# Kernel optimization log

Measured on AMD Instinct MI355X. Metric: run time of the kernel, lower is better.

Reference implementation:

```python
import jax, jax.numpy as jnp
import numpy as np

B, H1, H2, D, V1 = 4, 512, 640, 640, 1025  # V1 = vocab_size + 1 (blank)
T, U = 256, 128


def setup_inputs() -> dict:
    key = jax.random.key(0)
    ks = jax.random.split(key, 8)
    s = lambda fan_in: 1.0 / np.sqrt(fan_in)
    return {
        "encoder_outputs": jax.random.normal(ks[0], (B, H1, T), jnp.float32),
        "predictor_outputs": jax.random.normal(ks[1], (B, H2, U), jnp.float32),
        # Linear weights stored as [in, out]
        "W_enc": jax.random.uniform(ks[2], (H1, D), jnp.float32, -s(H1), s(H1)),
        "b_enc": jax.random.uniform(ks[3], (D,), jnp.float32, -s(H1), s(H1)),
        "W_pred": jax.random.uniform(ks[4], (H2, D), jnp.float32, -s(H2), s(H2)),
        "b_pred": jax.random.uniform(ks[5], (D,), jnp.float32, -s(H2), s(H2)),
        "W_out": jax.random.uniform(ks[6], (D, V1), jnp.float32, -s(D), s(D)),
        "b_out": jax.random.uniform(ks[7], (V1,), jnp.float32, -s(D), s(D)),
    }


def reference(encoder_outputs, predictor_outputs, W_enc, b_enc, W_pred, b_pred, W_out, b_out):
    # transpose(1,2): [B,H1,T] -> [B,T,H1], [B,H2,U] -> [B,U,H2], fused into einsum
    f = jnp.einsum("bht,hd->btd", encoder_outputs, W_enc) + b_enc   # [B,T,D]
    g = jnp.einsum("bhu,hd->bud", predictor_outputs, W_pred) + b_pred  # [B,U,D]
    h = jax.nn.relu(f[:, :, None, :] + g[:, None, :, :])            # [B,T,U,D]
    logits = jnp.einsum("btud,dv->btuv", h, W_out) + b_out          # [B,T,U,V+1]
    return jax.nn.log_softmax(logits, axis=-1)
```

## Files before the change

kernel.cpp:

```cpp
#include <hip/hip_runtime.h>
#include <hip/hip_bf16.h>

#define Bb 4
#define Tt 256
#define Uu 128
#define H1 512
#define H2 640
#define Dd 640
#define V1c 1025

typedef __bf16 bf16x8 __attribute__((ext_vector_type(8)));
typedef unsigned short ushort8 __attribute__((ext_vector_type(8)));
typedef unsigned short ushort4v __attribute__((ext_vector_type(4)));
typedef float floatx4 __attribute__((ext_vector_type(4)));

static __device__ __forceinline__ unsigned short f2bf(float x) {
    union { float f; unsigned u; } a; a.f = x;
    unsigned r = a.u + 0x7fffu + ((a.u >> 16) & 1u);
    return (unsigned short)(r >> 16);
}
static __device__ __forceinline__ float bf2f(unsigned short x) {
    union { unsigned u; float f; } a; a.u = ((unsigned)x) << 16; return a.f;
}

__global__ __launch_bounds__(640) void fg_fused(const float* __restrict__ enc,
                                                const float* __restrict__ Wenc,
                                                const float* __restrict__ benc,
                                                float* __restrict__ f,
                                                const float* __restrict__ pred,
                                                const float* __restrict__ Wpred,
                                                const float* __restrict__ bpred,
                                                float* __restrict__ g) {
    __shared__ float s[640 * 8];
    const bool isF = blockIdx.x < 128;
    const float* in   = isF ? enc : pred;
    const float* W    = isF ? Wenc : Wpred;
    const float* bias = isF ? benc : bpred;
    float* out        = isF ? f : g;
    const int H    = isF ? H1 : H2;
    const int Tdim = isF ? Tt : Uu;
    const int blk  = isF ? (int)blockIdx.x : (int)blockIdx.x - 128;
    const int tBlocks = Tdim >> 3;
    const int b  = blk / tBlocks;
    const int t0 = (blk % tBlocks) << 3;
    const float* inB = in + (size_t)b * H * Tdim + t0;
    const int tid = threadIdx.x;

    for (int h = tid; h < H; h += 640) {
        float4 v0 = *(const float4*)(inB + (size_t)h * Tdim);
        float4 v1 = *(const float4*)(inB + (size_t)h * Tdim + 4);
        *(float4*)(&s[h * 8])     = v0;
        *(float4*)(&s[h * 8 + 4]) = v1;
    }
    __syncthreads();

    const int d = tid;
    float acc[8];
    #pragma unroll
    for (int j = 0; j < 8; ++j) acc[j] = 0.f;
    #pragma unroll 4
    for (int h = 0; h < H; ++h) {
        float w = W[(size_t)h * Dd + d];
        float4 s0 = *(const float4*)(&s[h * 8]);
        float4 s1 = *(const float4*)(&s[h * 8 + 4]);
        acc[0] += s0.x * w; acc[1] += s0.y * w; acc[2] += s0.z * w; acc[3] += s0.w * w;
        acc[4] += s1.x * w; acc[5] += s1.y * w; acc[6] += s1.z * w; acc[7] += s1.w * w;
    }
    float bv = bias[d];
    float* o = out + ((size_t)b * Tdim + t0) * Dd + d;
    #pragma unroll
    for (int j = 0; j < 8; ++j) o[(size_t)j * Dd] = acc[j] + bv;
}

__global__ __launch_bounds__(256) void conv_wout2(const float* __restrict__ Wout,
                                                  unsigned short* __restrict__ Wb2,
                                                  float* __restrict__ wtail) {
    __shared__ float tile[32][128];
    const int blk = blockIdx.x;
    const int w = blk / 20;
    const int db = blk % 20;
    const int tid = threadIdx.x;

    #pragma unroll
    for (int i = 0; i < 16; ++i) {
        int idx = tid + 256 * i;
        int d_loc = idx >> 7;
        int v_loc = idx & 127;
        tile[d_loc][v_loc] = Wout[(size_t)(db * 32 + d_loc) * V1c + w * 128 + v_loc];
    }
    __syncthreads();

    #pragma unroll
    for (int k = 0; k < 2; ++k) {
        int gidx = tid * 2 + k;
        int nt  = gidx >> 6;
        int rem = gidx & 63;
        int l15 = rem >> 2;
        int lg  = rem & 3;
        int v_loc = nt * 16 + l15;
        ushort8 pk;
        #pragma unroll
        for (int j = 0; j < 8; ++j) pk[j] = f2bf(tile[lg * 8 + j][v_loc]);
        *(ushort8*)(Wb2 + (size_t)w * 81920 + db * 4096 + gidx * 8) = pk;
    }

    if (blk == 0) {
        for (int dd = tid; dd < Dd; dd += 256) wtail[dd] = Wout[(size_t)dd * V1c + 1024];
    }
}

__global__ __launch_bounds__(512, 2) void joint_main(const float* __restrict__ f,
                                                     const float* __restrict__ g,
                                                     const unsigned short* __restrict__ Wb2,
                                                     const float* __restrict__ wtail,
                                                     const float* __restrict__ b_out,
                                                     float* __restrict__ out) {
    __shared__ __align__(16) union UU {
        unsigned short hlds[2 * 64 * 328];
        float sOut[16 * 1025];
    } u;
    __shared__ float wtld[640];
    __shared__ float sPart[8 * 64];
    __shared__ float sRed[64];
    __shared__ float sTail[64];

    const int tid = threadIdx.x;
    const int l = tid & 63;
    const int w = tid >> 6;
    const int l15 = l & 15;
    const int lg = l >> 4;

    const int blk = blockIdx.x;
    const int uhalf = blk & 1;
    const int t = (blk >> 1) & 255;
    const int b = blk >> 9;
    const int u0 = uhalf * 64;
    const size_t fbase = ((size_t)b * Tt + t) * Dd;
    const size_t gbase = ((size_t)b * Uu + u0) * Dd;
    const size_t rowbase = (size_t)(b * Tt + t) * Uu + u0;

    for (int i = tid; i < Dd; i += 512) wtld[i] = wtail[i];

    floatx4 acc[4][8];
    #pragma unroll
    for (int i = 0; i < 4; ++i)
        #pragma unroll
        for (int j = 0; j < 8; ++j) acc[i][j] = (floatx4){0.f, 0.f, 0.f, 0.f};

    const unsigned short* __restrict__ bbase = Wb2 + (size_t)w * 81920 + (l15 * 32 + lg * 8);
    float tailAcc = 0.f;
    const int srow = w * 8 + (l >> 3);
    const int ssub = l & 7;

    {
        const int row = tid >> 3;
        const float* frow = f + fbase;
        const float* grow = g + gbase + (size_t)row * Dd;
        #pragma unroll
        for (int j = 0; j < 20; ++j) {
            int c4 = (tid & 7) + 8 * j;
            int d = c4 * 4;
            int half = (j >= 10) ? 1 : 0;
            int cloc = c4 - half * 80;
            float4 fv = *(const float4*)(frow + d);
            float4 gv = *(const float4*)(grow + d);
            float h0 = fv.x + gv.x; h0 = h0 > 0.f ? h0 : 0.f;
            float h1 = fv.y + gv.y; h1 = h1 > 0.f ? h1 : 0.f;
            float h2 = fv.z + gv.z; h2 = h2 > 0.f ? h2 : 0.f;
            float h3 = fv.w + gv.w; h3 = h3 > 0.f ? h3 : 0.f;
            ushort4v pk;
            pk.x = f2bf(h0); pk.y = f2bf(h1); pk.z = f2bf(h2); pk.w = f2bf(h3);
            *(ushort4v*)(&u.hlds[half * 20992 + row * 328 + cloc * 4]) = pk;
        }
    }
    __syncthreads();

    {
        ushort8 Bbuf[2][8];
        #pragma unroll
        for (int nt = 0; nt < 8; ++nt)
            Bbuf[0][nt] = *(const ushort8*)(bbase + nt * 512);
        #pragma unroll
        for (int ksg = 0; ksg < 20; ++ksg) {
            if (ksg < 19) {
                #pragma unroll
                for (int nt = 0; nt < 8; ++nt)
                    Bbuf[(ksg + 1) & 1][nt] =
                        *(const ushort8*)(bbase + (ksg + 1) * 4096 + nt * 512);
            }
            const int bufo = (ksg >= 10) ? 20992 : 0;
            const int ks = (ksg >= 10) ? (ksg - 10) : ksg;
            bf16x8 afrag[4];
            #pragma unroll
            for (int mt = 0; mt < 4; ++mt) {
                ushort8 av = *(const ushort8*)(&u.hlds[bufo + (mt * 16 + l15) * 328 + ks * 32 + lg * 8]);
                afrag[mt] = __builtin_bit_cast(bf16x8, av);
            }
            #pragma unroll
            for (int nt = 0; nt < 8; ++nt) {
                bf16x8 bfrag = __builtin_bit_cast(bf16x8, Bbuf[ksg & 1][nt]);
                #pragma unroll
                for (int mt = 0; mt < 4; ++mt) {
                    acc[mt][nt] = __builtin_amdgcn_mfma_f32_16x16x32_bf16(
                        afrag[mt], bfrag, acc[mt][nt], 0, 0, 0);
                }
            }
        }
    }

    #pragma unroll
    for (int j = 0; j < 20; ++j) {
        int c4 = ssub + 8 * j;
        int half = (j >= 10) ? 1 : 0;
        int cloc = c4 - half * 80;
        ushort4v hv = *(const ushort4v*)(&u.hlds[half * 20992 + srow * 328 + cloc * 4]);
        float4 wv = *(const float4*)(&wtld[c4 * 4]);
        tailAcc += bf2f(hv.x) * wv.x + bf2f(hv.y) * wv.y +
                   bf2f(hv.z) * wv.z + bf2f(hv.w) * wv.w;
    }

    tailAcc += __shfl_xor(tailAcc, 1);
    tailAcc += __shfl_xor(tailAcc, 2);
    tailAcc += __shfl_xor(tailAcc, 4);
    if (ssub == 0) sTail[srow] = tailAcc + b_out[1024];

    #pragma unroll
    for (int nt = 0; nt < 8; ++nt) {
        float bo = b_out[w * 128 + nt * 16 + l15];
        #pragma unroll
        for (int mt = 0; mt < 4; ++mt)
            #pragma unroll
            for (int r = 0; r < 4; ++r) acc[mt][nt][r] += bo;
    }

    #pragma unroll
    for (int mt = 0; mt < 4; ++mt) {
        #pragma unroll
        for (int r = 0; r < 4; ++r) {
            float m = acc[mt][0][r];
            #pragma unroll
            for (int nt = 1; nt < 8; ++nt) m = fmaxf(m, acc[mt][nt][r]);
            #pragma unroll
            for (int msk = 1; msk < 16; msk <<= 1) m = fmaxf(m, __shfl_xor(m, msk));
            if (l15 == 0) sPart[w * 64 + mt * 16 + lg * 4 + r] = m;
        }
    }
    __syncthreads();
    if (tid < 64) {
        float m = sTail[tid];
        #pragma unroll
        for (int ww = 0; ww < 8; ++ww) m = fmaxf(m, sPart[ww * 64 + tid]);
        sRed[tid] = m;
    }
    __syncthreads();

    #pragma unroll
    for (int mt = 0; mt < 4; ++mt) {
        #pragma unroll
        for (int r = 0; r < 4; ++r) {
            int row = mt * 16 + lg * 4 + r;
            float mx = sRed[row];
            float sv = 0.f;
            #pragma unroll
            for (int nt = 0; nt < 8; ++nt) sv += __expf(acc[mt][nt][r] - mx);
            #pragma unroll
            for (int msk = 1; msk < 16; msk <<= 1) sv += __shfl_xor(sv, msk);
            if (l15 == 0) sPart[w * 64 + row] = sv;
        }
    }
    __syncthreads();
    if (tid < 64) {
        float mx = sRed[tid];
        float sv = __expf(sTail[tid] - mx);
        #pragma unroll
        for (int ww = 0; ww < 8; ++ww) sv += sPart[ww * 64 + tid];
        sRed[tid] = mx + logf(sv);
    }
    __syncthreads();

    #pragma unroll
    for (int grp = 0; grp < 4; ++grp) {
        #pragma unroll
        for (int nt = 0; nt < 8; ++nt) {
            #pragma unroll
            for (int r = 0; r < 4; ++r) {
                u.sOut[(lg * 4 + r) * 1025 + w * 128 + nt * 16 + l15] =
                    acc[grp][nt][r] - sRed[grp * 16 + lg * 4 + r];
            }
        }
        if (tid < 16) u.sOut[tid * 1025 + 1024] = sTail[grp * 16 + tid] - sRed[grp * 16 + tid];
        __syncthreads();
        float* outp = out + (rowbase + grp * 16) * (size_t)V1c;
        #pragma unroll
        for (int k = 0; k < 8; ++k) {
            int i4 = tid + 512 * k;
            floatx4 v = *(const floatx4*)(&u.sOut[4 * i4]);
            __builtin_nontemporal_store(v, (floatx4*)(outp + 4 * i4));
        }
        if (tid < 4) {
            int i4 = tid + 4096;
            floatx4 v = *(const floatx4*)(&u.sOut[4 * i4]);
            __builtin_nontemporal_store(v, (floatx4*)(outp + 4 * i4));
        }
        __syncthreads();
    }
}

extern "C" void kernel_launch(void* const* d_in, const int* in_sizes, int n_in,
                              void* d_out, int out_size, void* d_ws, size_t ws_size,
                              hipStream_t stream) {
    const float* enc   = (const float*)d_in[0];
    const float* pred  = (const float*)d_in[1];
    const float* Wenc  = (const float*)d_in[2];
    const float* benc  = (const float*)d_in[3];
    const float* Wpred = (const float*)d_in[4];
    const float* bpred = (const float*)d_in[5];
    const float* Wout  = (const float*)d_in[6];
    const float* bout  = (const float*)d_in[7];

    float* f = (float*)d_ws;
    float* g = f + (size_t)Bb * Tt * Dd;
    unsigned short* Wb2 = (unsigned short*)(g + (size_t)Bb * Uu * Dd);
    float* wtail = (float*)(Wb2 + 8 * 81920);

    fg_fused<<<192, 640, 0, stream>>>(enc, Wenc, benc, f, pred, Wpred, bpred, g);
    conv_wout2<<<160, 256, 0, stream>>>(Wout, Wb2, wtail);
    joint_main<<<Bb * Tt * 2, 512, 0, stream>>>(f, g, Wb2, wtail, bout, (float*)d_out);
}
```

Before: 366.7 us.

## Merge prep kernels, fuse tail dot into h build, double-buffer output staging

Merges the f/g projection and W_out bf16 conversion kernels into one launch so their blocks run concurrently. In the joint kernel, the blank-column dot product is computed in fp32 while h is built, replacing a later pass that re-read bf16 h from LDS, and bf16 packing now uses the hardware v_cvt_pk_bf16_f32 instruction. Output staging is split into eight 8-row groups in two LDS buffers, so filling one group overlaps draining the previous and one barrier per group is removed. The tail value is now fp32-exact instead of bf16-rounded, and the smaller staging groups mean more, shorter store phases.

```diff
diff --git a/kernel.cpp b/kernel.cpp
--- a/kernel.cpp
+++ b/kernel.cpp
@@ -19,93 +19,90 @@
     unsigned r = a.u + 0x7fffu + ((a.u >> 16) & 1u);
     return (unsigned short)(r >> 16);
 }
-static __device__ __forceinline__ float bf2f(unsigned short x) {
-    union { unsigned u; float f; } a; a.u = ((unsigned)x) << 16; return a.f;
-}
-
-__global__ __launch_bounds__(640) void fg_fused(const float* __restrict__ enc,
-                                                const float* __restrict__ Wenc,
-                                                const float* __restrict__ benc,
-                                                float* __restrict__ f,
-                                                const float* __restrict__ pred,
-                                                const float* __restrict__ Wpred,
-                                                const float* __restrict__ bpred,
-                                                float* __restrict__ g) {
-    __shared__ float s[640 * 8];
-    const bool isF = blockIdx.x < 128;
-    const float* in   = isF ? enc : pred;
-    const float* W    = isF ? Wenc : Wpred;
-    const float* bias = isF ? benc : bpred;
-    float* out        = isF ? f : g;
-    const int H    = isF ? H1 : H2;
-    const int Tdim = isF ? Tt : Uu;
-    const int blk  = isF ? (int)blockIdx.x : (int)blockIdx.x - 128;
-    const int tBlocks = Tdim >> 3;
-    const int b  = blk / tBlocks;
-    const int t0 = (blk % tBlocks) << 3;
-    const float* inB = in + (size_t)b * H * Tdim + t0;
+static __device__ __forceinline__ unsigned cvt_pk_bf16(float lo, float hi) {
+    unsigned r;
+    asm("v_cvt_pk_bf16_f32 %0, %1, %2" : "=v"(r) : "v"(lo), "v"(hi));
+    return r;
+}
+
+__global__ __launch_bounds__(640) void prep(const float* __restrict__ enc,
+                                            const float* __restrict__ Wenc,
+                                            const float* __restrict__ benc,
+                                            float* __restrict__ f,
+                                            const float* __restrict__ pred,
+                                            const float* __restrict__ Wpred,
+                                            const float* __restrict__ bpred,
+                                            float* __restrict__ g,
+                                            const float* __restrict__ Wout,
+                                            unsigned short* __restrict__ Wb2,
+                                            float* __restrict__ wtail) {
+    __shared__ __align__(16) float sh[640 * 8];
     const int tid = threadIdx.x;
 
-    for (int h = tid; h < H; h += 640) {
-        float4 v0 = *(const float4*)(inB + (size_t)h * Tdim);
-        float4 v1 = *(const float4*)(inB + (size_t)h * Tdim + 4);
-        *(float4*)(&s[h * 8])     = v0;
-        *(float4*)(&s[h * 8 + 4]) = v1;
-    }
-    __syncthreads();
-
-    const int d = tid;
-    float acc[8];
-    #pragma unroll
-    for (int j = 0; j < 8; ++j) acc[j] = 0.f;
-    #pragma unroll 4
-    for (int h = 0; h < H; ++h) {
-        float w = W[(size_t)h * Dd + d];
-        float4 s0 = *(const float4*)(&s[h * 8]);
-        float4 s1 = *(const float4*)(&s[h * 8 + 4]);
-        acc[0] += s0.x * w; acc[1] += s0.y * w; acc[2] += s0.z * w; acc[3] += s0.w * w;
-        acc[4] += s1.x * w; acc[5] += s1.y * w; acc[6] += s1.z * w; acc[7] += s1.w * w;
-    }
-    float bv = bias[d];
-    float* o = out + ((size_t)b * Tdim + t0) * Dd + d;
-    #pragma unroll
-    for (int j = 0; j < 8; ++j) o[(size_t)j * Dd] = acc[j] + bv;
-}
-
-__global__ __launch_bounds__(256) void conv_wout2(const float* __restrict__ Wout,
-                                                  unsigned short* __restrict__ Wb2,
-                                                  float* __restrict__ wtail) {
-    __shared__ float tile[32][128];
-    const int blk = blockIdx.x;
-    const int w = blk / 20;
-    const int db = blk % 20;
-    const int tid = threadIdx.x;
-
-    #pragma unroll
-    for (int i = 0; i < 16; ++i) {
-        int idx = tid + 256 * i;
-        int d_loc = idx >> 7;
-        int v_loc = idx & 127;
-        tile[d_loc][v_loc] = Wout[(size_t)(db * 32 + d_loc) * V1c + w * 128 + v_loc];
-    }
-    __syncthreads();
-
-    #pragma unroll
-    for (int k = 0; k < 2; ++k) {
-        int gidx = tid * 2 + k;
-        int nt  = gidx >> 6;
-        int rem = gidx & 63;
-        int l15 = rem >> 2;
-        int lg  = rem & 3;
-        int v_loc = nt * 16 + l15;
-        ushort8 pk;
-        #pragma unroll
-        for (int j = 0; j < 8; ++j) pk[j] = f2bf(tile[lg * 8 + j][v_loc]);
-        *(ushort8*)(Wb2 + (size_t)w * 81920 + db * 4096 + gidx * 8) = pk;
-    }
-
-    if (blk == 0) {
-        for (int dd = tid; dd < Dd; dd += 256) wtail[dd] = Wout[(size_t)dd * V1c + 1024];
+    if (blockIdx.x < 192) {
+        const bool isF = blockIdx.x < 128;
+        const float* in   = isF ? enc : pred;
+        const float* W    = isF ? Wenc : Wpred;
+        const float* bias = isF ? benc : bpred;
+        float* out        = isF ? f : g;
+        const int H    = isF ? H1 : H2;
+        const int Tdim = isF ? Tt : Uu;
+        const int blk  = isF ? (int)blockIdx.x : (int)blockIdx.x - 128;
+        const int tBlocks = Tdim >> 3;
+        const int b  = blk / tBlocks;
+        const int t0 = (blk % tBlocks) << 3;
+        const float* inB = in + (size_t)b * H * Tdim + t0;
+
+        for (int h = tid; h < H; h += 640) {
+            float4 v0 = *(const float4*)(inB + (size_t)h * Tdim);
+            float4 v1 = *(const float4*)(inB + (size_t)h * Tdim + 4);
+            *(float4*)(&sh[h * 8])     = v0;
+            *(float4*)(&sh[h * 8 + 4]) = v1;
+        }
+        __syncthreads();
+
+        const int d = tid;
+        float acc[8];
+        #pragma unroll
+        for (int j = 0; j < 8; ++j) acc[j] = 0.f;
+        #pragma unroll 4
+        for (int h = 0; h < H; ++h) {
+            float w = W[(size_t)h * Dd + d];
+            float4 s0 = *(const float4*)(&sh[h * 8]);
+            float4 s1 = *(const float4*)(&sh[h * 8 + 4]);
+            acc[0] += s0.x * w; acc[1] += s0.y * w; acc[2] += s0.z * w; acc[3] += s0.w * w;
+            acc[4] += s1.x * w; acc[5] += s1.y * w; acc[6] += s1.z * w; acc[7] += s1.w * w;
+        }
+        float bv = bias[d];
+        float* o = out + ((size_t)b * Tdim + t0) * Dd + d;
+        #pragma unroll
+        for (int j = 0; j < 8; ++j) o[(size_t)j * Dd] = acc[j] + bv;
+    } else {
+        float (*tile)[129] = (float(*)[129])sh;
+        const int blk2 = blockIdx.x - 192;
+        const int w = blk2 / 20;
+        const int db = blk2 % 20;
+
+        for (int idx = tid; idx < 4096; idx += 640) {
+            int d_loc = idx >> 7;
+            int v_loc = idx & 127;
+            tile[d_loc][v_loc] = Wout[(size_t)(db * 32 + d_loc) * V1c + w * 128 + v_loc];
+        }
+        __syncthreads();
+
+        if (tid < 512) {
+            int gidx = tid;
+            int nt  = gidx >> 6;
+            int rem = gidx & 63;
+            int l15 = rem >> 2;
+            int lg  = rem & 3;
+            int v_loc = nt * 16 + l15;
+            ushort8 pk;
+            #pragma unroll
+            for (int j = 0; j < 8; ++j) pk[j] = f2bf(tile[lg * 8 + j][v_loc]);
+            *(ushort8*)(Wb2 + (size_t)w * 81920 + db * 4096 + gidx * 8) = pk;
+        }
+        if (blk2 == 0 && tid < Dd) wtail[tid] = Wout[(size_t)tid * V1c + 1024];
     }
 }
 
@@ -117,9 +114,8 @@
                                                      float* __restrict__ out) {
     __shared__ __align__(16) union UU {
         unsigned short hlds[2 * 64 * 328];
-        float sOut[16 * 1025];
+        float sOut[2 * 8 * 1025];
     } u;
-    __shared__ float wtld[640];
     __shared__ float sPart[8 * 64];
     __shared__ float sRed[64];
     __shared__ float sTail[64];
@@ -139,8 +135,6 @@
     const size_t gbase = ((size_t)b * Uu + u0) * Dd;
     const size_t rowbase = (size_t)(b * Tt + t) * Uu + u0;
 
-    for (int i = tid; i < Dd; i += 512) wtld[i] = wtail[i];
-
     floatx4 acc[4][8];
     #pragma unroll
     for (int i = 0; i < 4; ++i)
@@ -164,13 +158,16 @@
             int cloc = c4 - half * 80;
             float4 fv = *(const float4*)(frow + d);
             float4 gv = *(const float4*)(grow + d);
-            float h0 = fv.x + gv.x; h0 = h0 > 0.f ? h0 : 0.f;
-            float h1 = fv.y + gv.y; h1 = h1 > 0.f ? h1 : 0.f;
-            float h2 = fv.z + gv.z; h2 = h2 > 0.f ? h2 : 0.f;
-            float h3 = fv.w + gv.w; h3 = h3 > 0.f ? h3 : 0.f;
-            ushort4v pk;
-            pk.x = f2bf(h0); pk.y = f2bf(h1); pk.z = f2bf(h2); pk.w = f2bf(h3);
-            *(ushort4v*)(&u.hlds[half * 20992 + row * 328 + cloc * 4]) = pk;
+            float4 wv = *(const float4*)(wtail + d);
+            float h0 = fmaxf(fv.x + gv.x, 0.f);
+            float h1 = fmaxf(fv.y + gv.y, 0.f);
+            float h2 = fmaxf(fv.z + gv.z, 0.f);
+            float h3 = fmaxf(fv.w + gv.w, 0.f);
+            tailAcc += h0 * wv.x + h1 * wv.y + h2 * wv.z + h3 * wv.w;
+            uint2 pk;
+            pk.x = cvt_pk_bf16(h0, h1);
+            pk.y = cvt_pk_bf16(h2, h3);
+            *(uint2*)(&u.hlds[half * 20992 + row * 328 + cloc * 4]) = pk;
         }
     }
     __syncthreads();
@@ -208,17 +205,6 @@
         }
     }
 
-    #pragma unroll
-    for (int j = 0; j < 20; ++j) {
-        int c4 = ssub + 8 * j;
-        int half = (j >= 10) ? 1 : 0;
-        int cloc = c4 - half * 80;
-        ushort4v hv = *(const ushort4v*)(&u.hlds[half * 20992 + srow * 328 + cloc * 4]);
-        float4 wv = *(const float4*)(&wtld[c4 * 4]);
-        tailAcc += bf2f(hv.x) * wv.x + bf2f(hv.y) * wv.y +
-                   bf2f(hv.z) * wv.z + bf2f(hv.w) * wv.w;
-    }
-
     tailAcc += __shfl_xor(tailAcc, 1);
     tailAcc += __shfl_xor(tailAcc, 2);
     tailAcc += __shfl_xor(tailAcc, 4);
@@ -278,31 +264,53 @@
     }
     __syncthreads();
 
-    #pragma unroll
-    for (int grp = 0; grp < 4; ++grp) {
-        #pragma unroll
-        for (int nt = 0; nt < 8; ++nt) {
-            #pragma unroll
-            for (int r = 0; r < 4; ++r) {
-                u.sOut[(lg * 4 + r) * 1025 + w * 128 + nt * 16 + l15] =
-                    acc[grp][nt][r] - sRed[grp * 16 + lg * 4 + r];
-            }
-        }
-        if (tid < 16) u.sOut[tid * 1025 + 1024] = sTail[grp * 16 + tid] - sRed[grp * 16 + tid];
+    {
+        #define FILL(grp_)                                                            \
+        {                                                                             \
+            const int mt_ = (grp_) >> 1;                                              \
+            const int half8_ = (grp_) & 1;                                            \
+            float* buf_ = u.sOut + ((grp_) & 1) * 8200;                               \
+            if ((lg >> 1) == half8_) {                                                \
+                const int rl_ = (lg & 1) * 4;                                         \
+                _Pragma("unroll")                                                     \
+                for (int nt = 0; nt < 8; ++nt) {                                      \
+                    _Pragma("unroll")                                                 \
+                    for (int r = 0; r < 4; ++r) {                                     \
+                        buf_[(rl_ + r) * 1025 + w * 128 + nt * 16 + l15] =            \
+                            acc[mt_][nt][r] - sRed[(grp_) * 8 + rl_ + r];             \
+                    }                                                                 \
+                }                                                                     \
+            }                                                                         \
+            if (tid < 8) buf_[tid * 1025 + 1024] =                                    \
+                sTail[(grp_) * 8 + tid] - sRed[(grp_) * 8 + tid];                     \
+        }
+        #define DRAIN(grp_)                                                           \
+        {                                                                             \
+            const float* buf_ = u.sOut + ((grp_) & 1) * 8200;                         \
+            float* outp_ = out + (rowbase + (grp_) * 8) * (size_t)V1c;                \
+            _Pragma("unroll")                                                         \
+            for (int k = 0; k < 4; ++k) {                                             \
+                int i4 = tid + 512 * k;                                               \
+                floatx4 v = *(const floatx4*)(&buf_[4 * i4]);                         \
+                __builtin_nontemporal_store(v, (floatx4*)(outp_ + 4 * i4));           \
+            }                                                                         \
+            if (tid < 2) {                                                            \
+                int i4 = tid + 2048;                                                  \
+                floatx4 v = *(const floatx4*)(&buf_[4 * i4]);                         \
+                __builtin_nontemporal_store(v, (floatx4*)(outp_ + 4 * i4));           \
+            }                                                                         \
+        }
+        FILL(0);
         __syncthreads();
-        float* outp = out + (rowbase + grp * 16) * (size_t)V1c;
-        #pragma unroll
-        for (int k = 0; k < 8; ++k) {
-            int i4 = tid + 512 * k;
-            floatx4 v = *(const floatx4*)(&u.sOut[4 * i4]);
-            __builtin_nontemporal_store(v, (floatx4*)(outp + 4 * i4));
-        }
-        if (tid < 4) {
-            int i4 = tid + 4096;
-            floatx4 v = *(const floatx4*)(&u.sOut[4 * i4]);
-            __builtin_nontemporal_store(v, (floatx4*)(outp + 4 * i4));
-        }
-        __syncthreads();
+        #pragma unroll
+        for (int gg = 1; gg < 8; ++gg) {
+            FILL(gg);
+            DRAIN(gg - 1);
+            __syncthreads();
+        }
+        DRAIN(7);
+        #undef FILL
+        #undef DRAIN
     }
 }
 
@@ -323,7 +331,7 @@
     unsigned short* Wb2 = (unsigned short*)(g + (size_t)Bb * Uu * Dd);
     float* wtail = (float*)(Wb2 + 8 * 81920);
 
-    fg_fused<<<192, 640, 0, stream>>>(enc, Wenc, benc, f, pred, Wpred, bpred, g);
-    conv_wout2<<<160, 256, 0, stream>>>(Wout, Wb2, wtail);
+    prep<<<352, 640, 0, stream>>>(enc, Wenc, benc, f, pred, Wpred, bpred, g,
+                                  Wout, Wb2, wtail);
     joint_main<<<Bb * Tt * 2, 512, 0, stream>>>(f, g, Wb2, wtail, bout, (float*)d_out);
 }
```

Result: slower. 404.5 us (+10.3%).
